# Kernel tuning notes

Hardware: AMD Instinct MI355X
Metric: run time of the kernel (lower is better)

## Reference

```python
import jax, jax.numpy as jnp
import numpy as np

B, S, D = 64, 4096, 1024

def setup_inputs() -> dict:
    key = jax.random.key(0)
    k1, k2, k3 = jax.random.split(key, 3)
    inp = jax.random.normal(k1, (B, S, D), dtype=jnp.float32)
    lens = jax.random.randint(k2, (B,), 1, S + 1, dtype=jnp.int32)  # lengths in [1, S]
    w = jax.random.normal(k3, (1, D), dtype=jnp.float32) * (1.0 / np.sqrt(D))
    b = jnp.zeros((1,), dtype=jnp.float32)
    return {"inp": inp, "lens": lens, "w": w, "b": b}

def reference(inp, lens, w, b):
    # scores[b,s] = inp[b,s,:] @ w[0,:] + b
    scores = jnp.einsum("bsd,d->bs", inp, w[0]) + b[0]            # [B, S]
    mask = jnp.arange(inp.shape[1])[None, :] < lens[:, None]       # [B, S]
    scores = jnp.where(mask, scores, -jnp.inf)
    attn = jax.nn.softmax(scores, axis=1)                          # [B, S]
    context = jnp.einsum("bs,bsd->bd", attn, inp)                  # [B, D]
    return context
```

## Files before the change

kernel.cpp:

```cpp
#include <hip/hip_runtime.h>
#include <math.h>

#define BATCH 64
#define SEQ   4096
#define DIM   1024

__device__ __forceinline__ float dot16(const float4* x,
                                       const float4& w0, const float4& w1,
                                       const float4& w2, const float4& w3) {
    return x[0].x*w0.x + x[0].y*w0.y + x[0].z*w0.z + x[0].w*w0.w
         + x[1].x*w1.x + x[1].y*w1.y + x[1].z*w1.z + x[1].w*w1.w
         + x[2].x*w2.x + x[2].y*w2.y + x[2].z*w2.z + x[2].w*w2.w
         + x[3].x*w3.x + x[3].y*w3.y + x[3].z*w3.z + x[3].w*w3.w;
}

__global__ __launch_bounds__(256, 3)
void attn_partial_kernel(const float* __restrict__ inp,
                         const int*   __restrict__ lens,
                         const float* __restrict__ w,
                         float* __restrict__ ws_c,
                         float* __restrict__ ws_m,
                         float* __restrict__ ws_l,
                         int splits)
{
    const int split = blockIdx.x;
    const int b     = blockIdx.y;
    const int t     = threadIdx.x;
    const int wave  = t >> 6;
    const int lane  = t & 63;
    const int colb  = lane * 4;

    __shared__ float c_s[4][DIM];
    __shared__ float m_s[4];
    __shared__ float l_s[4];

    const int len   = lens[b];
    const int chunk = (len + splits - 1) / splits;
    const int s0    = split * chunk;
    const int s1    = min(s0 + chunk, len);

    const float4 w0 = *(const float4*)(w       + colb);
    const float4 w1 = *(const float4*)(w + 256 + colb);
    const float4 w2 = *(const float4*)(w + 512 + colb);
    const float4 w3 = *(const float4*)(w + 768 + colb);

    float  m = -INFINITY, l = 0.0f;
    float4 c[4] = {{0,0,0,0},{0,0,0,0},{0,0,0,0},{0,0,0,0}};

    const float* base = inp + (size_t)b * SEQ * DIM + colb;

    int r = s0 + (wave << 1);
    int pairs = 0;
    if (s1 - r >= 2) pairs = (s1 - r - 2) / 8 + 1;
    const int rs = r + pairs * 8;

    float4 xA[2][4], xB[2][4];

#define LOAD2(X, row_) do {                                                   \
        const float* rp_ = base + (size_t)(row_) * DIM;                       \
        _Pragma("unroll")                                                     \
        for (int j_ = 0; j_ < 2; ++j_)                                        \
            _Pragma("unroll")                                                 \
            for (int q_ = 0; q_ < 4; ++q_)                                    \
                X[j_][q_] = *(const float4*)(rp_ + j_ * DIM + q_ * 256);      \
    } while (0)

#define PROC2(X) do {                                                         \
        float pd0_ = dot16(X[0], w0, w1, w2, w3);                             \
        float pd1_ = dot16(X[1], w0, w1, w2, w3);                             \
        _Pragma("unroll")                                                     \
        for (int off_ = 32; off_ > 0; off_ >>= 1) {                           \
            pd0_ += __shfl_xor(pd0_, off_, 64);                               \
            pd1_ += __shfl_xor(pd1_, off_, 64);                               \
        }                                                                     \
        const float mn_    = fmaxf(m, fmaxf(pd0_, pd1_));                     \
        const float alpha_ = __expf(m - mn_);                                 \
        const float p0_    = __expf(pd0_ - mn_);                              \
        const float p1_    = __expf(pd1_ - mn_);                              \
        l = l * alpha_ + p0_ + p1_;                                           \
        _Pragma("unroll")                                                     \
        for (int q_ = 0; q_ < 4; ++q_) {                                      \
            c[q_].x = c[q_].x*alpha_ + p0_*X[0][q_].x + p1_*X[1][q_].x;       \
            c[q_].y = c[q_].y*alpha_ + p0_*X[0][q_].y + p1_*X[1][q_].y;       \
            c[q_].z = c[q_].z*alpha_ + p0_*X[0][q_].z + p1_*X[1][q_].z;       \
            c[q_].w = c[q_].w*alpha_ + p0_*X[0][q_].w + p1_*X[1][q_].w;       \
        }                                                                     \
        m = mn_;                                                              \
    } while (0)

    if (pairs > 0) LOAD2(xA, r);
    int p = 0;
    for (; p + 2 <= pairs; p += 2) {
        LOAD2(xB, r + 8);
        PROC2(xA);
        if (p + 2 < pairs) LOAD2(xA, r + 16);
        PROC2(xB);
        r += 16;
    }
    if (p < pairs) {
        PROC2(xA);
        r += 8;
    }

#undef LOAD2
#undef PROC2

    if (rs < s1) {
        const float* rp = base + (size_t)rs * DIM;
        const float4 x0 = *(const float4*)(rp);
        const float4 x1 = *(const float4*)(rp + 256);
        const float4 x2 = *(const float4*)(rp + 512);
        const float4 x3 = *(const float4*)(rp + 768);

        float pd = x0.x*w0.x + x0.y*w0.y + x0.z*w0.z + x0.w*w0.w
                 + x1.x*w1.x + x1.y*w1.y + x1.z*w1.z + x1.w*w1.w
                 + x2.x*w2.x + x2.y*w2.y + x2.z*w2.z + x2.w*w2.w
                 + x3.x*w3.x + x3.y*w3.y + x3.z*w3.z + x3.w*w3.w;
        #pragma unroll
        for (int off = 32; off > 0; off >>= 1)
            pd += __shfl_xor(pd, off, 64);

        const float mn    = fmaxf(m, pd);
        const float alpha = __expf(m - mn);
        const float pp    = __expf(pd - mn);
        l = l * alpha + pp;
        c[0].x = c[0].x*alpha + pp*x0.x;  c[0].y = c[0].y*alpha + pp*x0.y;
        c[0].z = c[0].z*alpha + pp*x0.z;  c[0].w = c[0].w*alpha + pp*x0.w;
        c[1].x = c[1].x*alpha + pp*x1.x;  c[1].y = c[1].y*alpha + pp*x1.y;
        c[1].z = c[1].z*alpha + pp*x1.z;  c[1].w = c[1].w*alpha + pp*x1.w;
        c[2].x = c[2].x*alpha + pp*x2.x;  c[2].y = c[2].y*alpha + pp*x2.y;
        c[2].z = c[2].z*alpha + pp*x2.z;  c[2].w = c[2].w*alpha + pp*x2.w;
        c[3].x = c[3].x*alpha + pp*x3.x;  c[3].y = c[3].y*alpha + pp*x3.y;
        c[3].z = c[3].z*alpha + pp*x3.z;  c[3].w = c[3].w*alpha + pp*x3.w;
        m = mn;
    }

    #pragma unroll
    for (int q = 0; q < 4; ++q)
        *(float4*)&c_s[wave][colb + q * 256] = c[q];
    if (lane == 0) { m_s[wave] = m; l_s[wave] = l; }
    __syncthreads();

    const float M = fmaxf(fmaxf(m_s[0], m_s[1]), fmaxf(m_s[2], m_s[3]));
    float sc[4];
    float L = 0.0f;
    #pragma unroll
    for (int iw = 0; iw < 4; ++iw) {
        sc[iw] = (m_s[iw] == -INFINITY) ? 0.0f : __expf(m_s[iw] - M);
        L += sc[iw] * l_s[iw];
    }

    const int oc = t * 4;
    float4 acc = {0,0,0,0};
    #pragma unroll
    for (int iw = 0; iw < 4; ++iw) {
        const float4 ci = *(const float4*)&c_s[iw][oc];
        acc.x += sc[iw]*ci.x; acc.y += sc[iw]*ci.y;
        acc.z += sc[iw]*ci.z; acc.w += sc[iw]*ci.w;
    }

    const size_t idx = (size_t)b * splits + split;
    *(float4*)(ws_c + idx * DIM + oc) = acc;
    if (t == 0) { ws_m[idx] = M; ws_l[idx] = L; }
}

__global__ __launch_bounds__(256)
void attn_reduce_kernel(const float* __restrict__ ws_c,
                        const float* __restrict__ ws_m,
                        const float* __restrict__ ws_l,
                        float* __restrict__ out, int splits)
{
    const int b  = blockIdx.x;
    const int t  = threadIdx.x;
    const int oc = t * 4;

    const float* mb = ws_m + (size_t)b * splits;
    const float* lb = ws_l + (size_t)b * splits;

    float M = -INFINITY;
    #pragma unroll 8
    for (int i = 0; i < splits; ++i) M = fmaxf(M, mb[i]);

    float  L   = 0.0f;
    float4 acc = {0,0,0,0};
    #pragma unroll 4
    for (int i = 0; i < splits; ++i) {
        const float mi  = mb[i];
        const float scl = (mi == -INFINITY) ? 0.0f : __expf(mi - M);
        L += scl * lb[i];
        const float4 ci = *(const float4*)(ws_c + ((size_t)b * splits + i) * DIM + oc);
        acc.x += scl*ci.x; acc.y += scl*ci.y;
        acc.z += scl*ci.z; acc.w += scl*ci.w;
    }
    const float inv = 1.0f / L;
    float4 o = { acc.x*inv, acc.y*inv, acc.z*inv, acc.w*inv };
    *(float4*)(out + (size_t)b * DIM + oc) = o;
}

extern "C" void kernel_launch(void* const* d_in, const int* in_sizes, int n_in,
                              void* d_out, int out_size, void* d_ws, size_t ws_size,
                              hipStream_t stream) {
    const float* inp  = (const float*)d_in[0];
    const int*   lens = (const int*)  d_in[1];
    const float* w    = (const float*)d_in[2];
    float* out = (float*)d_out;

    int splits = 64;
    while (splits > 1 &&
           (size_t)BATCH * splits * (DIM + 2) * sizeof(float) > ws_size)
        splits >>= 1;

    float* wsf  = (float*)d_ws;
    float* ws_c = wsf;
    float* ws_m = wsf + (size_t)BATCH * splits * DIM;
    float* ws_l = ws_m + (size_t)BATCH * splits;

    attn_partial_kernel<<<dim3(splits, BATCH), 256, 0, stream>>>(
        inp, lens, w, ws_c, ws_m, ws_l, splits);
    attn_reduce_kernel<<<BATCH, 256, 0, stream>>>(ws_c, ws_m, ws_l, out, splits);
}
```

Before: 1.239 ms.

## Triple-buffer row loads, double split count, and widen the reduce grid

The partial kernel now keeps three in-flight register buffers of row pairs instead of two, so two loads are outstanding while one pair is processed, to hide more memory latency. The number of sequence splits rises from 64 to 128 to put more blocks in flight. The reduce kernel is spread over a 4-by-batch grid with scalar per-column accumulation. The extra buffer raises register pressure under the three-blocks-per-SIMD launch bound and could cause spills. More splits also increase workspace traffic in the reduce step.

```diff
diff --git a/kernel.cpp b/kernel.cpp
--- a/kernel.cpp
+++ b/kernel.cpp
@@ -49,12 +49,12 @@
 
     const float* base = inp + (size_t)b * SEQ * DIM + colb;
 
-    int r = s0 + (wave << 1);
+    const int r0 = s0 + (wave << 1);
     int pairs = 0;
-    if (s1 - r >= 2) pairs = (s1 - r - 2) / 8 + 1;
-    const int rs = r + pairs * 8;
-
-    float4 xA[2][4], xB[2][4];
+    if (s1 - r0 >= 2) pairs = (s1 - r0 - 2) / 8 + 1;
+    const int rs = r0 + pairs * 8;
+
+    float4 xA[2][4], xB[2][4], xC[2][4];
 
 #define LOAD2(X, row_) do {                                                   \
         const float* rp_ = base + (size_t)(row_) * DIM;                       \
@@ -88,18 +88,21 @@
         m = mn_;                                                              \
     } while (0)
 
-    if (pairs > 0) LOAD2(xA, r);
-    int p = 0;
-    for (; p + 2 <= pairs; p += 2) {
-        LOAD2(xB, r + 8);
+    if (pairs > 0) LOAD2(xA, r0);
+    if (pairs > 1) LOAD2(xB, r0 + 8);
+    int p = 0, r = r0;
+    for (; p + 3 <= pairs; p += 3, r += 24) {
+        LOAD2(xC, r + 16);
         PROC2(xA);
-        if (p + 2 < pairs) LOAD2(xA, r + 16);
+        if (p + 4 <= pairs) LOAD2(xA, r + 24);
         PROC2(xB);
-        r += 16;
+        if (p + 5 <= pairs) LOAD2(xB, r + 32);
+        PROC2(xC);
     }
     if (p < pairs) {
         PROC2(xA);
-        r += 8;
+        ++p;
+        if (p < pairs) PROC2(xB);
     }
 
 #undef LOAD2
@@ -170,9 +173,10 @@
                         const float* __restrict__ ws_l,
                         float* __restrict__ out, int splits)
 {
-    const int b  = blockIdx.x;
+    const int q  = blockIdx.x;
+    const int b  = blockIdx.y;
     const int t  = threadIdx.x;
-    const int oc = t * 4;
+    const int col = q * 256 + t;
 
     const float* mb = ws_m + (size_t)b * splits;
     const float* lb = ws_l + (size_t)b * splits;
@@ -181,20 +185,16 @@
     #pragma unroll 8
     for (int i = 0; i < splits; ++i) M = fmaxf(M, mb[i]);
 
-    float  L   = 0.0f;
-    float4 acc = {0,0,0,0};
+    float L   = 0.0f;
+    float acc = 0.0f;
     #pragma unroll 4
     for (int i = 0; i < splits; ++i) {
         const float mi  = mb[i];
         const float scl = (mi == -INFINITY) ? 0.0f : __expf(mi - M);
         L += scl * lb[i];
-        const float4 ci = *(const float4*)(ws_c + ((size_t)b * splits + i) * DIM + oc);
-        acc.x += scl*ci.x; acc.y += scl*ci.y;
-        acc.z += scl*ci.z; acc.w += scl*ci.w;
-    }
-    const float inv = 1.0f / L;
-    float4 o = { acc.x*inv, acc.y*inv, acc.z*inv, acc.w*inv };
-    *(float4*)(out + (size_t)b * DIM + oc) = o;
+        acc += scl * ws_c[((size_t)b * splits + i) * DIM + col];
+    }
+    out[(size_t)b * DIM + col] = acc / L;
 }
 
 extern "C" void kernel_launch(void* const* d_in, const int* in_sizes, int n_in,
@@ -205,7 +205,7 @@
     const float* w    = (const float*)d_in[2];
     float* out = (float*)d_out;
 
-    int splits = 64;
+    int splits = 128;
     while (splits > 1 &&
            (size_t)BATCH * splits * (DIM + 2) * sizeof(float) > ws_size)
         splits >>= 1;
@@ -217,5 +217,6 @@
 
     attn_partial_kernel<<<dim3(splits, BATCH), 256, 0, stream>>>(
         inp, lens, w, ws_c, ws_m, ws_l, splits);
-    attn_reduce_kernel<<<BATCH, 256, 0, stream>>>(ws_c, ws_m, ws_l, out, splits);
-}
+    attn_reduce_kernel<<<dim3(4, BATCH), 256, 0, stream>>>(
+        ws_c, ws_m, ws_l, out, splits);
+}
```

New measurement: 1.290 ms. +4.1%, slower.
